# Optimization experiments

Hardware: AMD Instinct MI355X
Metric: run time of the kernel (lower is better)

## Reference

```python
import jax, jax.numpy as jnp
import numpy as np

B, H, W, C = 8, 64, 64, 64
C8 = C // 8

def setup_inputs() -> dict:
    key = jax.random.key(0)
    ks = jax.random.split(key, 5)
    x = jax.random.normal(ks[0], (B, H, W, C), dtype=jnp.float32)
    # 1x1 conv kernels (fan-in scaled) + biases
    wq = jax.random.normal(ks[1], (C, C8), dtype=jnp.float32) / np.sqrt(C)
    wk = jax.random.normal(ks[2], (C, C8), dtype=jnp.float32) / np.sqrt(C)
    wv = jax.random.normal(ks[3], (C, C), dtype=jnp.float32) / np.sqrt(C)
    bq = jnp.zeros((C8,), dtype=jnp.float32)
    bk = jnp.zeros((C8,), dtype=jnp.float32)
    bv = jnp.zeros((C,), dtype=jnp.float32)
    gamma = jax.random.normal(ks[4], (), dtype=jnp.float32)
    return {"x": x, "wq": wq, "bq": bq, "wk": wk, "bk": bk,
            "wv": wv, "bv": bv, "gamma": gamma}

def reference(x, wq, bq, wk, bk, wv, bv, gamma):
    b, h, w, c = x.shape
    n = h * w
    # 1x1 convs == per-pixel linear projections
    q = (jnp.einsum('bhwc,cd->bhwd', x, wq) + bq).reshape(b, n, -1)  # [B,N,C/8]
    k = (jnp.einsum('bhwc,cd->bhwd', x, wk) + bk).reshape(b, n, -1)  # [B,N,C/8]
    v = (jnp.einsum('bhwc,cd->bhwd', x, wv) + bv).reshape(b, n, -1)  # [B,N,C]
    # Unscaled attention: softmax over keys (last axis), no 1/sqrt(d)
    attn = jax.nn.softmax(jnp.einsum('bnd,bmd->bnm', q, k), axis=-1)  # [B,N,N]
    out = jnp.einsum('bnm,bmc->bnc', attn, v).reshape(b, h, w, c)
    return out * gamma + x
```

## Files before the change

kernel.cpp:

```cpp
#include <hip/hip_runtime.h>
#include <hip/hip_bf16.h>


#define BB 8
#define NN 4096
#define CC 64
#define PSTRIDE 72
#define LOG2E 1.44269504088896f

typedef _Float16 f16;
typedef _Float16 half8 __attribute__((ext_vector_type(8)));
typedef _Float16 half4 __attribute__((ext_vector_type(4)));
typedef float floatx4 __attribute__((ext_vector_type(4)));


__global__ __launch_bounds__(256) void proj_all_kernel(
    const float* __restrict__ x,
    const float* __restrict__ wq, const float* __restrict__ bq,
    const float* __restrict__ wk, const float* __restrict__ bk,
    const float* __restrict__ wv, const float* __restrict__ bv,
    f16* __restrict__ Qh, f16* __restrict__ Kf, f16* __restrict__ Vf)
{
    __shared__ alignas(16) f16 Ws[80][PSTRIDE];
    __shared__ float Bs[80];
    __shared__ alignas(16) f16 Vs[64][66];
    __shared__ alignas(16) f16 Ks[64][12];
    const int tid = threadIdx.x;

    for (int i = tid; i < 4096; i += 256) {
        int cin = i >> 6, cout = i & 63;
        Ws[cout][cin] = (f16)wv[i];
    }
    for (int i = tid; i < 512; i += 256) {
        int cin = i >> 3, c = i & 7;
        Ws[64 + c][cin] = (f16)(wq[i] * LOG2E);
        Ws[72 + c][cin] = (f16)wk[i];
    }
    if (tid < 80)
        Bs[tid] = (tid < 64) ? bv[tid]
                : (tid < 72 ? bq[tid - 64] * LOG2E : bk[tid - 72]);
    __syncthreads();

    const int wave = tid >> 6, lane = tid & 63;
    const int quad = lane >> 4, n16 = lane & 15;
    const long pb = (long)blockIdx.x * 64;
    const long p0 = pb + wave * 16;
    const int  b   = (int)(pb >> 12);
    const int  nnb = (int)(pb & 4095);

    half8 ax[2];
#pragma unroll
    for (int kh = 0; kh < 2; ++kh) {
        const float* xp = x + (p0 + n16) * 64 + kh * 32 + quad * 8;
        float4 x1 = *(const float4*)xp;
        float4 x2 = *(const float4*)(xp + 4);
        ax[kh][0] = (f16)x1.x; ax[kh][1] = (f16)x1.y;
        ax[kh][2] = (f16)x1.z; ax[kh][3] = (f16)x1.w;
        ax[kh][4] = (f16)x2.x; ax[kh][5] = (f16)x2.y;
        ax[kh][6] = (f16)x2.z; ax[kh][7] = (f16)x2.w;
    }

#pragma unroll
    for (int ct = 0; ct < 5; ++ct) {
        const int cout = (ct < 4) ? ct * 16 + n16 : 64 + n16;
        const float bias = Bs[cout];
        half8 b0 = *(const half8*)(&Ws[cout][quad * 8]);
        half8 b1 = *(const half8*)(&Ws[cout][32 + quad * 8]);
        floatx4 acc = {bias, bias, bias, bias};
        acc = __builtin_amdgcn_mfma_f32_16x16x32_f16(ax[0], b0, acc, 0, 0, 0);
        acc = __builtin_amdgcn_mfma_f32_16x16x32_f16(ax[1], b1, acc, 0, 0, 0);
        if (ct < 4) {
#pragma unroll
            for (int r = 0; r < 4; ++r)
                Vs[wave * 16 + quad * 4 + r][ct * 16 + n16] = (f16)acc[r];
        } else if (n16 < 8) {
            f16* dst = Qh + (p0 + quad * 4) * 8 + n16;
#pragma unroll
            for (int r = 0; r < 4; ++r) dst[r * 8] = (f16)acc[r];
        } else {
#pragma unroll
            for (int r = 0; r < 4; ++r)
                Ks[wave * 16 + quad * 4 + r][n16 - 8] = (f16)acc[r];
        }
    }
    __syncthreads();

#pragma unroll
    for (int u = 0; u < 2; ++u) {
        const int tt = wave * 2 + u;
        const int kb = tt >> 2, ct = tt & 3;
        half8 v;
#pragma unroll
        for (int j = 0; j < 8; ++j)
            v[j] = Vs[kb * 32 + quad * 8 + j][ct * 16 + n16];
        const size_t kbg = (size_t)b * 128 + (nnb >> 5) + kb;
        *(half8*)(Vf + (kbg * 4 + ct) * 512 + lane * 8) = v;
    }
    if (quad < 2) {
        half4 kv;
#pragma unroll
        for (int j = 0; j < 4; ++j)
            kv[j] = Ks[wave * 16 + n16][quad * 4 + j];
        const size_t kbg = (size_t)b * 256 + (nnb >> 4) + wave;
        *(half4*)(Kf + kbg * 128 + lane * 4) = kv;
    }
}

__global__ __launch_bounds__(256, 4) void attn_kernel(
    const f16* __restrict__ Qh, const f16* __restrict__ Kf,
    const f16* __restrict__ Vf,
    const float* __restrict__ x, const float* __restrict__ gptr,
    float* __restrict__ out)
{
    __shared__ alignas(16) f16 Pbuf[4 * 2 * 16 * PSTRIDE];
    __shared__ alignas(16) f16 Obuf[3][2][64][16];
    __shared__ float MLs[4][2][16][2];

    const int tid  = threadIdx.x;
    const int wave = tid >> 6, lane = tid & 63;
    const int quad = lane >> 4, n16 = lane & 15;
    const int ks = wave;

    const int b  = blockIdx.x & 7;
    const int qt = blockIdx.x >> 3;
    const size_t bN = (size_t)b * NN;

    half4 bq4[2];
#pragma unroll
    for (int qt2 = 0; qt2 < 2; ++qt2) {
#pragma unroll
        for (int j = 0; j < 4; ++j) bq4[qt2][j] = (f16)0.f;
        if (quad < 2)
            bq4[qt2] = *(const half4*)(Qh + (bN + qt * 32 + qt2 * 16 + n16) * 8 + quad * 4);
    }
    half4 ak[4];
#pragma unroll
    for (int t = 0; t < 4; ++t)
#pragma unroll
        for (int j = 0; j < 4; ++j) ak[t][j] = (f16)0.f;

    floatx4 oacc[2][4];
#pragma unroll
    for (int qt2 = 0; qt2 < 2; ++qt2)
#pragma unroll
        for (int ct = 0; ct < 4; ++ct) oacc[qt2][ct] = (floatx4){0.f, 0.f, 0.f, 0.f};
    float m_run[2] = {-1e30f, -1e30f}, l_loc[2] = {0.f, 0.f};

    const f16* kfb = Kf + ((size_t)b * 256 + ks * 64) * 128;
    const f16* vfb = Vf + ((size_t)b * 128 + ks * 32) * 2048;
    const floatx4 zero4 = {0.f, 0.f, 0.f, 0.f};
    f16* Pw0 = Pbuf + (wave * 2 + 0) * 16 * PSTRIDE;
    f16* Pw1 = Pbuf + (wave * 2 + 1) * 16 * PSTRIDE;

    for (int it = 0; it < 16; ++it) {
        if (quad < 2) {
#pragma unroll
            for (int t = 0; t < 4; ++t)
                ak[t] = *(const half4*)(kfb + (it * 4 + t) * 128 + lane * 4);
        }
        half8 av0[4];
#pragma unroll
        for (int ct = 0; ct < 4; ++ct)
            av0[ct] = *(const half8*)(vfb + ((size_t)(it * 2) * 4 + ct) * 512 + lane * 8);

        floatx4 sf[4];
#pragma unroll
        for (int t = 0; t < 4; ++t)
            sf[t] = __builtin_amdgcn_mfma_f32_16x16x16f16(ak[t], bq4[0], zero4, 0, 0, 0);

        half8 av1[4];
#pragma unroll
        for (int ct = 0; ct < 4; ++ct)
            av1[ct] = *(const half8*)(vfb + ((size_t)(it * 2 + 1) * 4 + ct) * 512 + lane * 8);

#pragma unroll
        for (int qt2 = 0; qt2 < 2; ++qt2) {
            if (qt2 == 1) {
#pragma unroll
                for (int t = 0; t < 4; ++t)
                    sf[t] = __builtin_amdgcn_mfma_f32_16x16x16f16(ak[t], bq4[1], zero4, 0, 0, 0);
            }
            float mx = sf[0][0];
#pragma unroll
            for (int t = 0; t < 4; ++t)
#pragma unroll
                for (int r = 0; r < 4; ++r) mx = fmaxf(mx, sf[t][r]);
            mx = fmaxf(mx, __shfl_xor(mx, 16, 64));
            mx = fmaxf(mx, __shfl_xor(mx, 32, 64));
            const float mnew = fmaxf(m_run[qt2], mx);
            const float alpha = __builtin_exp2f(m_run[qt2] - mnew);
            m_run[qt2] = mnew;
            float rs = 0.f;
#pragma unroll
            for (int t = 0; t < 4; ++t)
#pragma unroll
                for (int r = 0; r < 4; ++r) {
                    float pv = __builtin_exp2f(sf[t][r] - mnew);
                    sf[t][r] = pv;
                    rs += pv;
                }
            l_loc[qt2] = l_loc[qt2] * alpha + rs;
#pragma unroll
            for (int ct = 0; ct < 4; ++ct) oacc[qt2][ct] *= alpha;
            f16* Pw = qt2 ? Pw1 : Pw0;
#pragma unroll
            for (int t = 0; t < 4; ++t) {
                half4 pk;
#pragma unroll
                for (int r = 0; r < 4; ++r) pk[r] = (f16)sf[t][r];
                *(half4*)(Pw + n16 * PSTRIDE + t * 16 + quad * 4) = pk;
            }
        }
        __asm__ volatile("s_waitcnt lgkmcnt(0)" ::: "memory");

#pragma unroll
        for (int qt2 = 0; qt2 < 2; ++qt2) {
            f16* Pw = qt2 ? Pw1 : Pw0;
            half8 bp0 = *(const half8*)(Pw + n16 * PSTRIDE + quad * 8);
            half8 bp1 = *(const half8*)(Pw + n16 * PSTRIDE + 32 + quad * 8);
#pragma unroll
            for (int ct = 0; ct < 4; ++ct)
                oacc[qt2][ct] = __builtin_amdgcn_mfma_f32_16x16x32_f16(av0[ct], bp0, oacc[qt2][ct], 0, 0, 0);
#pragma unroll
            for (int ct = 0; ct < 4; ++ct)
                oacc[qt2][ct] = __builtin_amdgcn_mfma_f32_16x16x32_f16(av1[ct], bp1, oacc[qt2][ct], 0, 0, 0);
        }
    }

    float l_run[2];
#pragma unroll
    for (int qt2 = 0; qt2 < 2; ++qt2) {
        float l = l_loc[qt2];
        l += __shfl_xor(l, 16, 64);
        l += __shfl_xor(l, 32, 64);
        l_run[qt2] = l;
    }

    __syncthreads();
    if (ks > 0) {
#pragma unroll
        for (int qt2 = 0; qt2 < 2; ++qt2) {
            if (quad == 0) {
                MLs[ks][qt2][n16][0] = m_run[qt2];
                MLs[ks][qt2][n16][1] = l_run[qt2];
            }
            half8 p0, p1;
#pragma unroll
            for (int i = 0; i < 4; ++i) {
                p0[i]     = (f16)oacc[qt2][0][i];
                p0[4 + i] = (f16)oacc[qt2][1][i];
                p1[i]     = (f16)oacc[qt2][2][i];
                p1[4 + i] = (f16)oacc[qt2][3][i];
            }
            *(half8*)(&Obuf[ks - 1][qt2][lane][0]) = p0;
            *(half8*)(&Obuf[ks - 1][qt2][lane][8]) = p1;
        }
    }
    __syncthreads();
    if (ks == 0) {
        const float g = gptr[0];
#pragma unroll
        for (int qt2 = 0; qt2 < 2; ++qt2) {
            float m = m_run[qt2], l = l_run[qt2];
            float o[16];
#pragma unroll
            for (int ct = 0; ct < 4; ++ct)
#pragma unroll
                for (int r = 0; r < 4; ++r) o[ct * 4 + r] = oacc[qt2][ct][r];
#pragma unroll
            for (int p = 1; p < 4; ++p) {
                const float mp = MLs[p][qt2][n16][0];
                const float lp = MLs[p][qt2][n16][1];
                half8 q0 = *(const half8*)(&Obuf[p - 1][qt2][lane][0]);
                half8 q1 = *(const half8*)(&Obuf[p - 1][qt2][lane][8]);
                const float mn = fmaxf(m, mp);
                const float a1 = __builtin_exp2f(m - mn);
                const float a2 = __builtin_exp2f(mp - mn);
#pragma unroll
                for (int i = 0; i < 8; ++i) {
                    o[i]     = o[i] * a1 + (float)q0[i] * a2;
                    o[8 + i] = o[8 + i] * a1 + (float)q1[i] * a2;
                }
                l = l * a1 + lp * a2;
                m = mn;
            }
            const float scale = g / l;
            const int q = qt * 32 + qt2 * 16 + n16;
#pragma unroll
            for (int ct = 0; ct < 4; ++ct) {
                const size_t idx = (bN + q) * CC + ct * 16 + quad * 4;
                float4 xr = *(const float4*)(x + idx);
                float4 res;
                res.x = o[ct * 4 + 0] * scale + xr.x;
                res.y = o[ct * 4 + 1] * scale + xr.y;
                res.z = o[ct * 4 + 2] * scale + xr.z;
                res.w = o[ct * 4 + 3] * scale + xr.w;
                *(float4*)(out + idx) = res;
            }
        }
    }
}

extern "C" void kernel_launch(void* const* d_in, const int* in_sizes, int n_in,
                              void* d_out, int out_size, void* d_ws, size_t ws_size,
                              hipStream_t stream) {
    const float* x     = (const float*)d_in[0];
    const float* wq    = (const float*)d_in[1];
    const float* bq    = (const float*)d_in[2];
    const float* wk    = (const float*)d_in[3];
    const float* bk    = (const float*)d_in[4];
    const float* wv    = (const float*)d_in[5];
    const float* bv    = (const float*)d_in[6];
    const float* gamma = (const float*)d_in[7];
    float* out = (float*)d_out;

    f16* Qh = (f16*)d_ws;
    f16* Kf = Qh + (size_t)BB * NN * 8;
    f16* Vf = Kf + (size_t)BB * 256 * 128;

    proj_all_kernel<<<512, 256, 0, stream>>>(x, wq, bq, wk, bk, wv, bv, Qh, Kf, Vf);
    attn_kernel<<<BB * 128, 256, 0, stream>>>(Qh, Kf, Vf, x, gamma, out);
}
```

Measured before the change: 131.6 us.

## Split attention key range across eight waves and alias Obuf onto Pbuf

The attention kernel now runs 512 threads per block, so eight waves each handle one eighth of the keys (8 iterations instead of 16). The final merge combines seven partial results instead of three. Shared memory is unified so the partial-output buffer aliases the P staging buffer to keep LDS use bounded. P packing switches to the packed round-toward-zero convert intrinsic, and the V staging pitch in the projection kernel changes to 68. The changes add more parallelism per query tile but lengthen the serial merge done by wave 0 and raise register pressure against the new launch bound.

After: 520.8 us. +295.6%, slower.

```diff
diff --git a/kernel.cpp b/kernel.cpp
--- a/kernel.cpp
+++ b/kernel.cpp
@@ -11,7 +11,17 @@
 typedef _Float16 f16;
 typedef _Float16 half8 __attribute__((ext_vector_type(8)));
 typedef _Float16 half4 __attribute__((ext_vector_type(4)));
+typedef __fp16 fp16x2 __attribute__((ext_vector_type(2)));
 typedef float floatx4 __attribute__((ext_vector_type(4)));
+
+static __device__ inline half4 pack4(float a, float b, float c, float d) {
+    fp16x2 lo = __builtin_amdgcn_cvt_pkrtz(a, b);
+    fp16x2 hi = __builtin_amdgcn_cvt_pkrtz(c, d);
+    unsigned int lou = __builtin_bit_cast(unsigned int, lo);
+    unsigned int hiu = __builtin_bit_cast(unsigned int, hi);
+    unsigned long long packed = (unsigned long long)lou | ((unsigned long long)hiu << 32);
+    return __builtin_bit_cast(half4, packed);
+}
 
 
 __global__ __launch_bounds__(256) void proj_all_kernel(
@@ -23,7 +33,7 @@
 {
     __shared__ alignas(16) f16 Ws[80][PSTRIDE];
     __shared__ float Bs[80];
-    __shared__ alignas(16) f16 Vs[64][66];
+    __shared__ alignas(16) f16 Vs[64][68];
     __shared__ alignas(16) f16 Ks[64][12];
     const int tid = threadIdx.x;
 
@@ -106,15 +116,16 @@
     }
 }
 
-__global__ __launch_bounds__(256, 4) void attn_kernel(
+__global__ __launch_bounds__(512, 8) void attn_kernel(
     const f16* __restrict__ Qh, const f16* __restrict__ Kf,
     const f16* __restrict__ Vf,
     const float* __restrict__ x, const float* __restrict__ gptr,
     float* __restrict__ out)
 {
-    __shared__ alignas(16) f16 Pbuf[4 * 2 * 16 * PSTRIDE];
-    __shared__ alignas(16) f16 Obuf[3][2][64][16];
-    __shared__ float MLs[4][2][16][2];
+    __shared__ alignas(16) char smem[8 * 2 * 16 * PSTRIDE * 2 + 2048];
+    f16*   Pbuf = (f16*)smem;
+    f16*   Obuf = (f16*)smem;
+    float* MLs  = (float*)(smem + 8 * 2 * 16 * PSTRIDE * 2);
 
     const int tid  = threadIdx.x;
     const int wave = tid >> 6, lane = tid & 63;
@@ -146,13 +157,13 @@
         for (int ct = 0; ct < 4; ++ct) oacc[qt2][ct] = (floatx4){0.f, 0.f, 0.f, 0.f};
     float m_run[2] = {-1e30f, -1e30f}, l_loc[2] = {0.f, 0.f};
 
-    const f16* kfb = Kf + ((size_t)b * 256 + ks * 64) * 128;
-    const f16* vfb = Vf + ((size_t)b * 128 + ks * 32) * 2048;
+    const f16* kfb = Kf + ((size_t)b * 256 + ks * 32) * 128;
+    const f16* vfb = Vf + ((size_t)b * 128 + ks * 16) * 2048;
     const floatx4 zero4 = {0.f, 0.f, 0.f, 0.f};
     f16* Pw0 = Pbuf + (wave * 2 + 0) * 16 * PSTRIDE;
     f16* Pw1 = Pbuf + (wave * 2 + 1) * 16 * PSTRIDE;
 
-    for (int it = 0; it < 16; ++it) {
+    for (int it = 0; it < 8; ++it) {
         if (quad < 2) {
 #pragma unroll
             for (int t = 0; t < 4; ++t)
@@ -205,9 +216,7 @@
             f16* Pw = qt2 ? Pw1 : Pw0;
 #pragma unroll
             for (int t = 0; t < 4; ++t) {
-                half4 pk;
-#pragma unroll
-                for (int r = 0; r < 4; ++r) pk[r] = (f16)sf[t][r];
+                half4 pk = pack4(sf[t][0], sf[t][1], sf[t][2], sf[t][3]);
                 *(half4*)(Pw + n16 * PSTRIDE + t * 16 + quad * 4) = pk;
             }
         }
@@ -241,8 +250,8 @@
 #pragma unroll
         for (int qt2 = 0; qt2 < 2; ++qt2) {
             if (quad == 0) {
-                MLs[ks][qt2][n16][0] = m_run[qt2];
-                MLs[ks][qt2][n16][1] = l_run[qt2];
+                MLs[((ks * 2 + qt2) * 16 + n16) * 2 + 0] = m_run[qt2];
+                MLs[((ks * 2 + qt2) * 16 + n16) * 2 + 1] = l_run[qt2];
             }
             half8 p0, p1;
 #pragma unroll
@@ -252,8 +261,9 @@
                 p1[i]     = (f16)oacc[qt2][2][i];
                 p1[4 + i] = (f16)oacc[qt2][3][i];
             }
-            *(half8*)(&Obuf[ks - 1][qt2][lane][0]) = p0;
-            *(half8*)(&Obuf[ks - 1][qt2][lane][8]) = p1;
+            f16* ob = Obuf + (((ks - 1) * 2 + qt2) * 64 + lane) * 16;
+            *(half8*)(ob)     = p0;
+            *(half8*)(ob + 8) = p1;
         }
     }
     __syncthreads();
@@ -267,12 +277,12 @@
             for (int ct = 0; ct < 4; ++ct)
 #pragma unroll
                 for (int r = 0; r < 4; ++r) o[ct * 4 + r] = oacc[qt2][ct][r];
-#pragma unroll
-            for (int p = 1; p < 4; ++p) {
-                const float mp = MLs[p][qt2][n16][0];
-                const float lp = MLs[p][qt2][n16][1];
-                half8 q0 = *(const half8*)(&Obuf[p - 1][qt2][lane][0]);
-                half8 q1 = *(const half8*)(&Obuf[p - 1][qt2][lane][8]);
+            for (int p = 1; p < 8; ++p) {
+                const float mp = MLs[((p * 2 + qt2) * 16 + n16) * 2 + 0];
+                const float lp = MLs[((p * 2 + qt2) * 16 + n16) * 2 + 1];
+                const f16* ob = Obuf + (((p - 1) * 2 + qt2) * 64 + lane) * 16;
+                half8 q0 = *(const half8*)(ob);
+                half8 q1 = *(const half8*)(ob + 8);
                 const float mn = fmaxf(m, mp);
                 const float a1 = __builtin_exp2f(m - mn);
                 const float a2 = __builtin_exp2f(mp - mn);
@@ -319,5 +329,5 @@
     f16* Vf = Kf + (size_t)BB * 256 * 128;
 
     proj_all_kernel<<<512, 256, 0, stream>>>(x, wq, bq, wk, bk, wv, bv, Qh, Kf, Vf);
-    attn_kernel<<<BB * 128, 256, 0, stream>>>(Qh, Kf, Vf, x, gamma, out);
+    attn_kernel<<<BB * 128, 512, 0, stream>>>(Qh, Kf, Vf, x, gamma, out);
 }
```
